# Performance work log

Hardware: AMD Instinct MI355X
Metric: run time of the kernel (lower is better)

The kernel has to match this reference:

```python
import jax, jax.numpy as jnp
import numpy as np

B, L, W = 64, 20, 48
D = W * W           # 2304, MoE input/output size (image_width**2)
E = 4               # num_experts
HID = 2 * D         # expert hidden size
K = 1               # top_k
LOSS_COEF = 1e-2


def _cv_squared(x):
    # torch: x.var() (unbiased) / (x.mean()**2 + eps)
    eps = 1e-10
    return jnp.var(x, ddof=1) / (jnp.mean(x) ** 2 + eps)


def _moe(x, w_gate, w1, b1, w2, b2):
    # Noisy top-k gating, inference path (train=False => clean logits, no noise).
    logits = x @ w_gate                                   # [B, E]
    top_logits, top_idx = jax.lax.top_k(logits, K + 1)    # min(k+1, E)
    topk_gates = jax.nn.softmax(top_logits[:, :K], axis=-1)
    gates = jnp.zeros_like(logits).at[
        jnp.arange(x.shape[0])[:, None], top_idx[:, :K]
    ].set(topk_gates)                                     # [B, E] sparse gates
    importance = gates.sum(0)
    load = (gates > 0).sum(0).astype(x.dtype)             # _gates_to_load
    aux = LOSS_COEF * (_cv_squared(importance) + _cv_squared(load))
    # Dense expert compute weighted by gates (same math as dispatch/combine).
    h = jax.nn.relu(jnp.einsum('bd,edh->beh', x, w1) + b1)      # [B,E,HID]
    y = jnp.einsum('beh,ehd->bed', h, w2) + b2                  # [B,E,D]
    out = jnp.einsum('be,bed->bd', gates, y)                    # [B,D]
    return out, aux


def _conv3d(x, w, b, pad):
    y = jax.lax.conv_general_dilated(
        x, w, window_strides=(1, 1, 1), padding=pad,
        dimension_numbers=('NCDHW', 'OIDHW', 'NCDHW'))
    return y + b[None, :, None, None, None]


def _forward(input, conv1_w, conv1_b, conv2_w, conv2_b,
             t_gate, t_w1, t_b1, t_w2, t_b2,
             a_gate, a_w1, a_b1, a_w2, a_b2,
             q_gate, q_w1, q_b1, q_w2, q_b2,
             enc_w, enc_b, dec_w, dec_b):
    x = jnp.transpose(input, (0, 2, 1, 3, 4))                   # [B,1,L,H,W]
    x = jax.nn.relu(_conv3d(x, conv1_w, conv1_b, ((1, 1), (1, 1), (1, 1))))
    x = jax.nn.relu(_conv3d(x, conv2_w, conv2_b, ((0, 0), (1, 1), (1, 1))))  # [B,1,1,H,W]
    xf = x.reshape(x.shape[0], -1)                              # [B, D]
    transform, l1 = _moe(xf, t_gate, t_w1, t_b1, t_w2, t_b2)
    add, l2 = _moe(xf, a_gate, a_w1, a_b1, a_w2, a_b2)
    quad, l3 = _moe(xf, q_gate, q_w1, q_b1, q_w2, q_b2)
    s = input.shape                                             # [B,L,1,H,W]
    transform = transform.reshape(s[0], 1, s[2], s[3], s[4])
    add = add.reshape(s[0], 1, s[2], s[3], s[4])
    quad = quad.reshape(s[0], 1, s[2], s[3], s[4])
    out = input * input * quad + input * transform + add        # [B,L,1,H,W]
    # encoder = Linear(D,D)+ReLU, decoder = Linear(D,D) over flattened H*W
    of = out.reshape(s[0], s[1], D)
    of = jax.nn.relu(of @ enc_w + enc_b)
    of = of @ dec_w + dec_b
    of = jax.nn.sigmoid(of)
    return of.reshape(s), l1 + l2 + l3


def setup_inputs() -> dict:
    key = jax.random.key(0)
    ks = jax.random.split(key, 32)
    sc = 0.02
    inp = {
        'input': jax.random.normal(ks[0], (B, L, 1, W, W), jnp.float32),
        'conv1_w': jax.random.normal(ks[1], (10, 1, 3, 3, 3), jnp.float32) * sc,
        'conv1_b': jnp.zeros((10,), jnp.float32),
        'conv2_w': jax.random.normal(ks[2], (1, 10, L, 3, 3), jnp.float32) * sc,
        'conv2_b': jnp.zeros((1,), jnp.float32),
        'enc_w': jax.random.normal(ks[3], (D, D), jnp.float32) * sc,
        'enc_b': jnp.zeros((D,), jnp.float32),
        'dec_w': jax.random.normal(ks[4], (D, D), jnp.float32) * sc,
        'dec_b': jnp.zeros((D,), jnp.float32),
    }
    for i, p in enumerate(['t', 'a', 'q']):
        k0, k1, k2 = jax.random.split(ks[5 + i], 3)
        inp[p + '_gate'] = jnp.zeros((D, E), jnp.float32) + jax.random.normal(k0, (D, E), jnp.float32) * sc
        inp[p + '_w1'] = jax.random.normal(k1, (E, D, HID), jnp.float32) * sc
        inp[p + '_b1'] = jnp.zeros((E, HID), jnp.float32)
        inp[p + '_w2'] = jax.random.normal(k2, (E, HID, D), jnp.float32) * sc
        inp[p + '_b2'] = jnp.zeros((E, D), jnp.float32)
    return inp


def reference(input, conv1_w, conv1_b, conv2_w, conv2_b,
              t_gate, t_w1, t_b1, t_w2, t_b2,
              a_gate, a_w1, a_b1, a_w2, a_b2,
              q_gate, q_w1, q_b1, q_w2, q_b2,
              enc_w, enc_b, dec_w, dec_b):
    return _forward(input, conv1_w, conv1_b, conv2_w, conv2_b,
                    t_gate, t_w1, t_b1, t_w2, t_b2,
                    a_gate, a_w1, a_b1, a_w2, a_b2,
                    q_gate, q_w1, q_b1, q_w2, q_b2,
                    enc_w, enc_b, dec_w, dec_b)
```

## Files before the change

kernel.cpp:

```cpp
#include <hip/hip_runtime.h>
#include <stdint.h>

#define NB 64
#define NL 20
#define ND 2304
#define NE 4
#define NH 4608
#define NM 1280

typedef float f32x4 __attribute__((ext_vector_type(4)));
typedef __bf16 bf16x8 __attribute__((ext_vector_type(8)));
typedef unsigned short u16;
typedef u16 u16x4 __attribute__((ext_vector_type(4)));
typedef unsigned int u32;
typedef u32 u32x4 __attribute__((ext_vector_type(4)));

__device__ __forceinline__ u16 f2bf(float f) {
  u32 u = __builtin_bit_cast(u32, f);
  u += 0x7fffu + ((u >> 16) & 1u);
  return (u16)(u >> 16);
}

__device__ __forceinline__ void gl_lds16(const void* g, void* l) {
  __builtin_amdgcn_global_load_lds(
      (const __attribute__((address_space(1))) void*)g,
      (__attribute__((address_space(3))) void*)l, 16, 0, 0);
}

#define OFF_XFACC 0
#define OFF_XF    147456
#define OFF_H     294912
#define OFF_Y     1179648
#define OFF_AUX   1622016
#define OFF_CNT   1622020
#define OFF_ROWS  1622032
#define OFF_OFB   1622240
#define OFF_H1B   3096800
#define OFF_ENCWB 4571360
#define OFF_DECWB 7225568
#define OFF_XC    9879776
#define OFF_P     10322144

__global__ __launch_bounds__(256) void k_zero(float* __restrict__ p) {
  p[(size_t)blockIdx.x * 256 + threadIdx.x] = 0.f;
}

__global__ __launch_bounds__(256) void k_conv(
    const float* __restrict__ in, const float* __restrict__ w1,
    const float* __restrict__ b1, const float* __restrict__ w2,
    float* __restrict__ xf_acc) {
  __shared__ float insl[3][50][50];
  __shared__ float c1[2][50][50];
  __shared__ float w1s[270];
  __shared__ float w2s[90];
  __shared__ float b1s[10];
  const int d = blockIdx.x, b = blockIdx.y, t = threadIdx.x;
  for (int i = t; i < 270; i += 256) w1s[i] = w1[i];
  for (int i = t; i < 90; i += 256) w2s[i] = w2[(size_t)((i / 9) * 20 + d) * 9 + (i % 9)];
  if (t < 10) b1s[t] = b1[t];
  for (int i = t; i < 7500; i += 256) {
    int s = i / 2500, rr = (i % 2500) / 50, cc = i % 50;
    int gd = d - 1 + s, gy = rr - 1, gx = cc - 1;
    float v = 0.f;
    if (gd >= 0 && gd < NL && (unsigned)gy < 48u && (unsigned)gx < 48u)
      v = in[((size_t)b * NL + gd) * ND + gy * 48 + gx];
    insl[s][rr][cc] = v;
  }
  for (int i = t; i < 5000; i += 256) ((float*)c1)[i] = 0.f;
  float s2[3][4];
#pragma unroll
  for (int qi = 0; qi < 3; ++qi)
#pragma unroll
    for (int xq = 0; xq < 4; ++xq) s2[qi][xq] = 0.f;
  __syncthreads();
  for (int pc = 0; pc < 5; ++pc) {
#pragma unroll
    for (int qi = 0; qi < 3; ++qi) {
      int q = t + qi * 256;
      if (q < 576) {
        int y = q / 12, x0 = (q % 12) * 4;
        float a0[4], a1[4];
        const float bb0 = b1s[2 * pc], bb1 = b1s[2 * pc + 1];
#pragma unroll
        for (int xq = 0; xq < 4; ++xq) { a0[xq] = bb0; a1[xq] = bb1; }
#pragma unroll
        for (int kd = 0; kd < 3; ++kd)
#pragma unroll
          for (int ky = 0; ky < 3; ++ky) {
            float v[6];
#pragma unroll
            for (int i = 0; i < 6; ++i) v[i] = insl[kd][y + ky][x0 + i];
            const float* wa = &w1s[(2 * pc) * 27 + kd * 9 + ky * 3];
            const float* wb = wa + 27;
#pragma unroll
            for (int xq = 0; xq < 4; ++xq) {
              a0[xq] += v[xq] * wa[0] + v[xq + 1] * wa[1] + v[xq + 2] * wa[2];
              a1[xq] += v[xq] * wb[0] + v[xq + 1] * wb[1] + v[xq + 2] * wb[2];
            }
          }
#pragma unroll
        for (int xq = 0; xq < 4; ++xq) {
          c1[0][y + 1][x0 + 1 + xq] = fmaxf(a0[xq], 0.f);
          c1[1][y + 1][x0 + 1 + xq] = fmaxf(a1[xq], 0.f);
        }
      }
    }
    __syncthreads();
#pragma unroll
    for (int qi = 0; qi < 3; ++qi) {
      int q = t + qi * 256;
      if (q < 576) {
        int y = q / 12, x0 = (q % 12) * 4;
#pragma unroll
        for (int cc = 0; cc < 2; ++cc) {
#pragma unroll
          for (int ky = 0; ky < 3; ++ky) {
            float v[6];
#pragma unroll
            for (int i = 0; i < 6; ++i) v[i] = c1[cc][y + ky][x0 + i];
            const float* wr = &w2s[(2 * pc + cc) * 9 + ky * 3];
#pragma unroll
            for (int xq = 0; xq < 4; ++xq)
              s2[qi][xq] += v[xq] * wr[0] + v[xq + 1] * wr[1] + v[xq + 2] * wr[2];
          }
        }
      }
    }
    __syncthreads();
  }
#pragma unroll
  for (int qi = 0; qi < 3; ++qi) {
    int q = t + qi * 256;
    if (q < 576) {
#pragma unroll
      for (int xq = 0; xq < 4; ++xq)
        atomicAdd(&xf_acc[(size_t)b * ND + q * 4 + xq], s2[qi][xq]);
    }
  }
}

__global__ __launch_bounds__(256) void k_bias_relu(
    const float* __restrict__ acc, const float* __restrict__ c2b, float* __restrict__ xf) {
  size_t i = (size_t)blockIdx.x * 256 + threadIdx.x;
  xf[i] = fmaxf(acc[i] + c2b[0], 0.f);
}

__global__ __launch_bounds__(256) void k_gate(
    const float* __restrict__ xf,
    const float* __restrict__ g0, const float* __restrict__ g1, const float* __restrict__ g2,
    float* __restrict__ aux, int* __restrict__ cnt, int* __restrict__ rows) {
  const int p = blockIdx.x, t = threadIdx.x;
  const float* __restrict__ g = (p == 0) ? g0 : ((p == 1) ? g1 : g2);
  __shared__ float lg[64][4];
  __shared__ int lidx[64];
  __shared__ int lcnt[4];
  if (t < 4) lcnt[t] = 0;
  const int wv = t >> 6, l = t & 63;
  for (int b0 = 0; b0 < 64; b0 += 4) {
    int bb = b0 + wv;
    f32x4 acc = {0.f, 0.f, 0.f, 0.f};
    const float* xr = xf + (size_t)bb * ND + l * 36;
    const float* gr = g + (size_t)l * 36 * 4;
#pragma unroll
    for (int i4 = 0; i4 < 9; ++i4) {
      f32x4 xv = *(const f32x4*)(xr + i4 * 4);
#pragma unroll
      for (int qq = 0; qq < 4; ++qq) {
        f32x4 gv = *(const f32x4*)(gr + (i4 * 4 + qq) * 4);
        acc += xv[qq] * gv;
      }
    }
#pragma unroll
    for (int e = 0; e < 4; ++e) {
      float pv = acc[e];
#pragma unroll
      for (int off = 32; off > 0; off >>= 1) pv += __shfl_down(pv, off);
      if (l == 0) lg[bb][e] = pv;
    }
  }
  __syncthreads();
  if (t < 64) {
    float best = lg[t][0];
    int bi = 0;
#pragma unroll
    for (int e = 1; e < 4; ++e)
      if (lg[t][e] > best) { best = lg[t][e]; bi = e; }
    lidx[t] = bi;
    atomicAdd(&lcnt[bi], 1);
  }
  __syncthreads();
  if (t == 0) {
    int ofs[4]; int run = 0;
#pragma unroll
    for (int e = 0; e < 4; ++e) { ofs[e] = run; run += lcnt[e]; cnt[p * 4 + e] = lcnt[e]; }
    for (int b = 0; b < 64; ++b) { int e = lidx[b]; rows[p * 64 + ofs[e]++] = b; }
    float var = 0.f;
#pragma unroll
    for (int e = 0; e < 4; ++e) { float dd = (float)lcnt[e] - 16.f; var += dd * dd; }
    var *= (1.f / 3.f);
    aux[p] = 0.02f * var / (256.f + 1e-10f);
  }
}

__global__ __launch_bounds__(256) void k_gather(
    const float* __restrict__ xf, const int* __restrict__ rows, u16* __restrict__ Xb) {
  const int slot = blockIdx.x, t = threadIdx.x;
  const int r = rows[slot];
  const f32x4* src = (const f32x4*)(xf + (size_t)r * ND);
  u16x4* dst = (u16x4*)(Xb + (size_t)slot * ND);
  for (int i = t; i < ND / 4; i += 256) {
    f32x4 v = src[i];
    u16x4 o;
#pragma unroll
    for (int q = 0; q < 4; ++q) o[q] = f2bf(v[q]);
    dst[i] = o;
  }
}

template <int K, int N, int KS>
__global__ __launch_bounds__(256) void k_moe_mfma(
    const u16* __restrict__ Xb,
    const float* __restrict__ wt, const float* __restrict__ wa, const float* __restrict__ wq,
    const int* __restrict__ cnt, float* __restrict__ P) {
  constexpr int KL = K / KS;
  constexpr int NT = KL / 32;
  const int tile = blockIdx.x;
  const int ks = blockIdx.y;
  const int pe = blockIdx.z >> 1, ch = blockIdx.z & 1;
  const int p = pe >> 2, e = pe & 3;
  const int c = cnt[p * 4 + e];
  const int rstart = ch * 32;
  if (rstart >= c) return;
  const int nrows = min(32, c - rstart);
  int pref = 0;
  for (int e2 = 0; e2 < e; ++e2) pref += cnt[p * 4 + e2];
  const int slot0 = p * 64 + pref + rstart;
  const float* __restrict__ W = (p == 0) ? wt : ((p == 1) ? wa : wq);
  __shared__ float wb[4][32 * 64];
  const int t = threadIdx.x;
  const int w = t >> 6, l = t & 63;
  const int l15 = l & 15, l4 = l >> 4;
  const int mbase = (w & 1) * 16;
  const int nb0 = (w >> 1) * 32;

  int ar = slot0 + mbase + l15; if (ar > 191) ar = 191;
  const u16* Ag = Xb + (size_t)ar * K + ks * KL + l4 * 8;
  bf16x8 areg[NT];
#pragma unroll
  for (int kt = 0; kt < NT; ++kt) areg[kt] = *(const bf16x8*)(Ag + kt * 32);

  const float* Wg = W + (size_t)e * K * N + (size_t)(ks * KL) * N + tile * 64;
#define STAGEW(BUF, KT)                                                       \
  { _Pragma("unroll")                                                         \
    for (int j = 0; j < 2; ++j)                                               \
      gl_lds16(Wg + ((size_t)((KT) * 32 + w * 8 + j * 4 + l4)) * N + l15 * 4, \
               &wb[BUF][(w * 8 + j * 4) * 64]); }

  f32x4 acc[2] = {};

  STAGEW(0, 0); STAGEW(1, 1); STAGEW(2, 2);
  asm volatile("s_waitcnt vmcnt(0)" ::: "memory");
  __syncthreads();

#pragma unroll
  for (int kt = 0; kt < NT; ++kt) {
    if (kt + 3 < NT) STAGEW((kt + 3) & 3, kt + 3);
    const float* ww = &wb[kt & 3][0];
#pragma unroll
    for (int i = 0; i < 2; ++i) {
      const int nb = nb0 + i * 16 + l15;
      bf16x8 bfr;
#pragma unroll
      for (int j = 0; j < 8; ++j)
        bfr[j] = (__bf16)ww[(l4 * 8 + j) * 64 + nb];
      acc[i] = __builtin_amdgcn_mfma_f32_16x16x32_bf16(areg[kt], bfr, acc[i], 0, 0, 0);
    }
    if (kt + 3 < NT)      { asm volatile("s_waitcnt vmcnt(4)" ::: "memory"); }
    else if (kt + 2 < NT) { asm volatile("s_waitcnt vmcnt(2)" ::: "memory"); }
    else if (kt + 1 < NT) { asm volatile("s_waitcnt vmcnt(0)" ::: "memory"); }
    __syncthreads();
  }
#undef STAGEW

  const size_t pbase = (size_t)ks * 192 * N;
#pragma unroll
  for (int i = 0; i < 2; ++i) {
    const int n = tile * 64 + nb0 + i * 16 + l15;
#pragma unroll
    for (int r = 0; r < 4; ++r) {
      const int m = mbase + l4 * 4 + r;
      if (m < nrows) P[pbase + (size_t)(slot0 + m) * N + n] = acc[i][r];
    }
  }
}

__global__ __launch_bounds__(256) void k_red1(
    const float* __restrict__ P,
    const float* __restrict__ b1t, const float* __restrict__ b1a, const float* __restrict__ b1q,
    const int* __restrict__ cnt, u16* __restrict__ Hb) {
  const int slot = blockIdx.y;
  const int p = slot >> 6, pos = slot & 63;
  int e = 0, run = cnt[p * 4];
  while (pos >= run && e < 3) { ++e; run += cnt[p * 4 + e]; }
  const float* __restrict__ b1 = (p == 0) ? b1t : ((p == 1) ? b1a : b1q);
  const int j0 = blockIdx.x * 1024 + threadIdx.x * 4;
  if (j0 >= NH) return;
  f32x4 s = *(const f32x4*)(b1 + (size_t)e * NH + j0);
#pragma unroll
  for (int ks = 0; ks < 8; ++ks)
    s += *(const f32x4*)(P + ((size_t)ks * 192 + slot) * NH + j0);
  u16x4 o;
#pragma unroll
  for (int q = 0; q < 4; ++q) o[q] = f2bf(fmaxf(s[q], 0.f));
  *(u16x4*)(Hb + (size_t)slot * NH + j0) = o;
}

__global__ __launch_bounds__(256) void k_red2(
    const float* __restrict__ P,
    const float* __restrict__ b2t, const float* __restrict__ b2a, const float* __restrict__ b2q,
    const int* __restrict__ cnt, const int* __restrict__ rows, float* __restrict__ Y) {
  const int slot = blockIdx.y;
  const int p = slot >> 6, pos = slot & 63;
  int e = 0, run = cnt[p * 4];
  while (pos >= run && e < 3) { ++e; run += cnt[p * 4 + e]; }
  const float* __restrict__ b2 = (p == 0) ? b2t : ((p == 1) ? b2a : b2q);
  const int b = rows[slot];
  const int t = threadIdx.x;
  if (t >= 192) return;
  const int j0 = blockIdx.x * 768 + t * 4;
  f32x4 s = *(const f32x4*)(b2 + (size_t)e * ND + j0);
#pragma unroll
  for (int ks = 0; ks < 16; ++ks)
    s += *(const f32x4*)(P + ((size_t)ks * 192 + slot) * ND + j0);
  *(f32x4*)(Y + (size_t)(p * 64 + b) * ND + j0) = s;
}

__global__ __launch_bounds__(256) void k_combine(
    const float* __restrict__ in, const float* __restrict__ Y, u16* __restrict__ ofb) {
  const size_t i = (size_t)blockIdx.x * 256 + threadIdx.x;
  const size_t e0 = i * 4;
  const int row = (int)(e0 / ND);
  const int d = (int)(e0 - (size_t)row * ND);
  const int b = row / NL;
  f32x4 v = *(const f32x4*)(in + e0);
  const size_t yb = (size_t)b * ND + d;
  f32x4 tt = *(const f32x4*)(Y + yb);
  f32x4 aa = *(const f32x4*)(Y + (size_t)64 * ND + yb);
  f32x4 qq = *(const f32x4*)(Y + (size_t)128 * ND + yb);
  u16x4 o;
#pragma unroll
  for (int q = 0; q < 4; ++q) {
    float f = v[q] * v[q] * qq[q] + v[q] * tt[q] + aa[q];
    o[q] = f2bf(f);
  }
  *(u16x4*)(ofb + e0) = o;
}

__global__ __launch_bounds__(256) void k_wt(
    const float* __restrict__ encw, const float* __restrict__ decw,
    u16* __restrict__ encb, u16* __restrict__ decb) {
  __shared__ float tl[32][33];
  const float* __restrict__ src = blockIdx.z ? decw : encw;
  u16* __restrict__ dst = blockIdx.z ? decb : encb;
  const int k0 = blockIdx.x * 32, n0 = blockIdx.y * 32;
  const int tx = threadIdx.x & 31, ty = threadIdx.x >> 5;
  for (int r = ty; r < 32; r += 8) tl[r][tx] = src[(size_t)(k0 + r) * ND + n0 + tx];
  __syncthreads();
  for (int r = ty; r < 32; r += 8) dst[(size_t)(n0 + r) * ND + k0 + tx] = f2bf(tl[tx][r]);
}

template <int MODE>
__global__ __launch_bounds__(256) void k_gemm(
    const u16* __restrict__ A, const u16* __restrict__ Bt,
    const float* __restrict__ bias, void* __restrict__ outp,
    const float* __restrict__ aux) {
  __shared__ u16 As[64 * 32];
  __shared__ u16 Bs[128 * 32];
  const int t = threadIdx.x;
  const int bm = blockIdx.x, bn = blockIdx.y;
  const int lane = t & 63;
  const int wr = (t >> 7) & 1, wc = (t >> 6) & 1;
  const int l15 = lane & 15, l4 = lane >> 4;
  f32x4 acc[2][4] = {};
  const int r0 = t >> 2, kc0 = (t & 3) * 8;
  const int r1 = (t + 256) >> 2, kc1 = ((t + 256) & 3) * 8;
  const size_t baseA = (size_t)(bm * 64) * ND;
  const size_t baseB = (size_t)(bn * 128) * ND;
  for (int k0 = 0; k0 < ND; k0 += 32) {
    *(u32x4*)(As + t * 8) = *(const u32x4*)(A + baseA + (size_t)r0 * ND + k0 + kc0);
    *(u32x4*)(Bs + t * 8) = *(const u32x4*)(Bt + baseB + (size_t)r0 * ND + k0 + kc0);
    *(u32x4*)(Bs + (t + 256) * 8) = *(const u32x4*)(Bt + baseB + (size_t)r1 * ND + k0 + kc1);
    __syncthreads();
    bf16x8 af[2], bfr[4];
#pragma unroll
    for (int i = 0; i < 2; ++i)
      af[i] = *(const bf16x8*)(As + (wr * 32 + i * 16 + l15) * 32 + l4 * 8);
#pragma unroll
    for (int i = 0; i < 4; ++i)
      bfr[i] = *(const bf16x8*)(Bs + (wc * 64 + i * 16 + l15) * 32 + l4 * 8);
#pragma unroll
    for (int mi = 0; mi < 2; ++mi)
#pragma unroll
      for (int ni = 0; ni < 4; ++ni)
        acc[mi][ni] = __builtin_amdgcn_mfma_f32_16x16x32_bf16(af[mi], bfr[ni], acc[mi][ni], 0, 0, 0);
    __syncthreads();
  }
  const int colbase = bn * 128 + wc * 64;
  const int rowbase = bm * 64 + wr * 32;
#pragma unroll
  for (int mi = 0; mi < 2; ++mi) {
#pragma unroll
    for (int ni = 0; ni < 4; ++ni) {
      const int colg = colbase + ni * 16 + l15;
      const float bv = bias[colg];
#pragma unroll
      for (int r = 0; r < 4; ++r) {
        const int rowg = rowbase + mi * 16 + l4 * 4 + r;
        float v = acc[mi][ni][r] + bv;
        if (MODE == 0) {
          ((u16*)outp)[(size_t)rowg * ND + colg] = f2bf(fmaxf(v, 0.f));
        } else {
          ((float*)outp)[(size_t)rowg * ND + colg] = 1.f / (1.f + __expf(-v));
        }
      }
    }
  }
  if (MODE == 1 && bm == 0 && bn == 0 && t == 0)
    ((float*)outp)[(size_t)NM * ND] = aux[0] + aux[1] + aux[2];
}

extern "C" void kernel_launch(void* const* d_in, const int* in_sizes, int n_in,
                              void* d_out, int out_size, void* d_ws, size_t ws_size,
                              hipStream_t stream) {
  (void)in_sizes; (void)n_in; (void)out_size; (void)ws_size;
  const float* input   = (const float*)d_in[0];
  const float* conv1_w = (const float*)d_in[1];
  const float* conv1_b = (const float*)d_in[2];
  const float* conv2_w = (const float*)d_in[3];
  const float* conv2_b = (const float*)d_in[4];
  const float* enc_w   = (const float*)d_in[5];
  const float* enc_b   = (const float*)d_in[6];
  const float* dec_w   = (const float*)d_in[7];
  const float* dec_b   = (const float*)d_in[8];
  const float* gate_t = (const float*)d_in[9];
  const float* w1_t   = (const float*)d_in[10];
  const float* b1_t   = (const float*)d_in[11];
  const float* w2_t   = (const float*)d_in[12];
  const float* b2_t   = (const float*)d_in[13];
  const float* gate_a = (const float*)d_in[14];
  const float* w1_a   = (const float*)d_in[15];
  const float* b1_a   = (const float*)d_in[16];
  const float* w2_a   = (const float*)d_in[17];
  const float* b2_a   = (const float*)d_in[18];
  const float* gate_q = (const float*)d_in[19];
  const float* w1_q   = (const float*)d_in[20];
  const float* b1_q   = (const float*)d_in[21];
  const float* w2_q   = (const float*)d_in[22];
  const float* b2_q   = (const float*)d_in[23];

  float* ws = (float*)d_ws;
  float* xf_acc = ws + OFF_XFACC;
  float* xf     = ws + OFF_XF;
  u16*   Hb     = (u16*)(ws + OFF_H);
  float* Y      = ws + OFF_Y;
  float* aux    = ws + OFF_AUX;
  int*   cnt    = (int*)(ws + OFF_CNT);
  int*   rows   = (int*)(ws + OFF_ROWS);
  u16*   ofb    = (u16*)(ws + OFF_OFB);
  u16*   h1b    = (u16*)(ws + OFF_H1B);
  u16*   encwb  = (u16*)(ws + OFF_ENCWB);
  u16*   decwb  = (u16*)(ws + OFF_DECWB);
  u16*   Xcb    = (u16*)(ws + OFF_XC);
  float* P      = ws + OFF_P;

  k_zero<<<576, 256, 0, stream>>>(xf_acc);
  k_conv<<<dim3(20, 64), 256, 0, stream>>>(input, conv1_w, conv1_b, conv2_w, xf_acc);
  k_bias_relu<<<576, 256, 0, stream>>>(xf_acc, conv2_b, xf);
  k_wt<<<dim3(72, 72, 2), 256, 0, stream>>>(enc_w, dec_w, encwb, decwb);
  k_gate<<<3, 256, 0, stream>>>(xf, gate_t, gate_a, gate_q, aux, cnt, rows);
  k_gather<<<192, 256, 0, stream>>>(xf, rows, Xcb);
  k_moe_mfma<ND, NH, 8><<<dim3(72, 8, 24), 256, 0, stream>>>(Xcb, w1_t, w1_a, w1_q, cnt, P);
  k_red1<<<dim3(5, 192), 256, 0, stream>>>(P, b1_t, b1_a, b1_q, cnt, Hb);
  k_moe_mfma<NH, ND, 16><<<dim3(36, 16, 24), 256, 0, stream>>>(Hb, w2_t, w2_a, w2_q, cnt, P);
  k_red2<<<dim3(3, 192), 256, 0, stream>>>(P, b2_t, b2_a, b2_q, cnt, rows, Y);
  k_combine<<<2880, 256, 0, stream>>>(input, Y, ofb);
  k_gemm<0><<<dim3(20, 18), 256, 0, stream>>>(ofb, encwb, enc_b, (void*)h1b, aux);
  k_gemm<1><<<dim3(20, 18), 256, 0, stream>>>(h1b, decwb, dec_b, d_out, aux);
}
```

Baseline: 527.0 us.

## Load MoE expert weights directly into registers instead of staging through LDS

Removes the LDS ring buffer and global_load_lds staging for the fp32 expert weights in the MoE MFMA kernel. Each lane now loads its own weight column values straight into registers with a two-buffer software prefetch. A-fragments are also loaded per iteration instead of being preloaded into a register array. This drops the LDS round trip and the per-step barriers and waitcnts. In exchange the global loads are scalar 4-byte loads with a large row stride, so coalescing is poorer, and the code assumes NT is odd.

```diff
diff --git a/kernel.cpp b/kernel.cpp
--- a/kernel.cpp
+++ b/kernel.cpp
@@ -19,12 +19,6 @@
   u32 u = __builtin_bit_cast(u32, f);
   u += 0x7fffu + ((u >> 16) & 1u);
   return (u16)(u >> 16);
-}
-
-__device__ __forceinline__ void gl_lds16(const void* g, void* l) {
-  __builtin_amdgcn_global_load_lds(
-      (const __attribute__((address_space(1))) void*)g,
-      (__attribute__((address_space(3))) void*)l, 16, 0, 0);
 }
 
 #define OFF_XFACC 0
@@ -236,7 +230,6 @@
   for (int e2 = 0; e2 < e; ++e2) pref += cnt[p * 4 + e2];
   const int slot0 = p * 64 + pref + rstart;
   const float* __restrict__ W = (p == 0) ? wt : ((p == 1) ? wa : wq);
-  __shared__ float wb[4][32 * 64];
   const int t = threadIdx.x;
   const int w = t >> 6, l = t & 63;
   const int l15 = l & 15, l4 = l >> 4;
@@ -245,42 +238,41 @@
 
   int ar = slot0 + mbase + l15; if (ar > 191) ar = 191;
   const u16* Ag = Xb + (size_t)ar * K + ks * KL + l4 * 8;
-  bf16x8 areg[NT];
-#pragma unroll
-  for (int kt = 0; kt < NT; ++kt) areg[kt] = *(const bf16x8*)(Ag + kt * 32);
-
-  const float* Wg = W + (size_t)e * K * N + (size_t)(ks * KL) * N + tile * 64;
-#define STAGEW(BUF, KT)                                                       \
+
+  const float* Wg = W + (size_t)e * K * N + (size_t)(ks * KL + l4 * 8) * N
+                      + tile * 64 + nb0 + l15;
+
+  float wA[16], wB[16];
+  f32x4 acc[2] = {};
+
+#define LOADW(BUF, KT)                                                        \
   { _Pragma("unroll")                                                         \
-    for (int j = 0; j < 2; ++j)                                               \
-      gl_lds16(Wg + ((size_t)((KT) * 32 + w * 8 + j * 4 + l4)) * N + l15 * 4, \
-               &wb[BUF][(w * 8 + j * 4) * 64]); }
-
-  f32x4 acc[2] = {};
-
-  STAGEW(0, 0); STAGEW(1, 1); STAGEW(2, 2);
-  asm volatile("s_waitcnt vmcnt(0)" ::: "memory");
-  __syncthreads();
-
-#pragma unroll
-  for (int kt = 0; kt < NT; ++kt) {
-    if (kt + 3 < NT) STAGEW((kt + 3) & 3, kt + 3);
-    const float* ww = &wb[kt & 3][0];
-#pragma unroll
-    for (int i = 0; i < 2; ++i) {
-      const int nb = nb0 + i * 16 + l15;
-      bf16x8 bfr;
-#pragma unroll
-      for (int j = 0; j < 8; ++j)
-        bfr[j] = (__bf16)ww[(l4 * 8 + j) * 64 + nb];
-      acc[i] = __builtin_amdgcn_mfma_f32_16x16x32_bf16(areg[kt], bfr, acc[i], 0, 0, 0);
-    }
-    if (kt + 3 < NT)      { asm volatile("s_waitcnt vmcnt(4)" ::: "memory"); }
-    else if (kt + 2 < NT) { asm volatile("s_waitcnt vmcnt(2)" ::: "memory"); }
-    else if (kt + 1 < NT) { asm volatile("s_waitcnt vmcnt(0)" ::: "memory"); }
-    __syncthreads();
-  }
-#undef STAGEW
+    for (int i = 0; i < 2; ++i)                                               \
+      _Pragma("unroll")                                                       \
+      for (int j = 0; j < 8; ++j)                                             \
+        BUF[i * 8 + j] = Wg[(size_t)((KT) * 32 + j) * N + i * 16]; }
+
+#define DO_MFMA(BUF, AF)                                                      \
+  { _Pragma("unroll")                                                         \
+    for (int i = 0; i < 2; ++i) {                                             \
+      bf16x8 bfr;                                                             \
+      _Pragma("unroll")                                                       \
+      for (int j = 0; j < 8; ++j) bfr[j] = (__bf16)BUF[i * 8 + j];            \
+      acc[i] = __builtin_amdgcn_mfma_f32_16x16x32_bf16(AF, bfr, acc[i], 0, 0, 0); \
+    } }
+
+  LOADW(wA, 0);
+#pragma unroll 1
+  for (int pr = 0; pr < (NT - 1) / 2; ++pr) {
+    const int kt = pr * 2;
+    LOADW(wB, kt + 1);
+    { bf16x8 a0 = *(const bf16x8*)(Ag + kt * 32); DO_MFMA(wA, a0); }
+    LOADW(wA, kt + 2);
+    { bf16x8 a1 = *(const bf16x8*)(Ag + (kt + 1) * 32); DO_MFMA(wB, a1); }
+  }
+  { bf16x8 a8 = *(const bf16x8*)(Ag + (NT - 1) * 32); DO_MFMA(wA, a8); }
+#undef LOADW
+#undef DO_MFMA
 
   const size_t pbase = (size_t)ks * 192 * N;
 #pragma unroll
```

Result: slower. 598.0 us (+13.5%).

## Replace conv atomics with per-depth partials and prefetch all MoE weight tiles

Applied to the files above, without the earlier changes.

The conv kernel now writes a separate partial sum for each depth slice into scratch, and the bias-relu kernel adds the 20 partials. This removes the zero-init kernel and the float atomics. The MoE MFMA kernel now issues every K-tile weight load up front into padded LDS buffers, one per tile, and waits on them one by one with decreasing vmcnt. This replaces the 4-deep ring buffer and removes the per-iteration restaging, in exchange for more LDS per block and a hardcoded wait sequence that assumes NT=9.

```diff
diff --git a/kernel.cpp b/kernel.cpp
--- a/kernel.cpp
+++ b/kernel.cpp
@@ -41,14 +41,10 @@
 #define OFF_XC    9879776
 #define OFF_P     10322144
 
-__global__ __launch_bounds__(256) void k_zero(float* __restrict__ p) {
-  p[(size_t)blockIdx.x * 256 + threadIdx.x] = 0.f;
-}
-
 __global__ __launch_bounds__(256) void k_conv(
     const float* __restrict__ in, const float* __restrict__ w1,
     const float* __restrict__ b1, const float* __restrict__ w2,
-    float* __restrict__ xf_acc) {
+    float* __restrict__ xfp) {
   __shared__ float insl[3][50][50];
   __shared__ float c1[2][50][50];
   __shared__ float w1s[270];
@@ -132,17 +128,19 @@
   for (int qi = 0; qi < 3; ++qi) {
     int q = t + qi * 256;
     if (q < 576) {
-#pragma unroll
-      for (int xq = 0; xq < 4; ++xq)
-        atomicAdd(&xf_acc[(size_t)b * ND + q * 4 + xq], s2[qi][xq]);
+      f32x4 o = {s2[qi][0], s2[qi][1], s2[qi][2], s2[qi][3]};
+      *(f32x4*)(xfp + ((size_t)d * NB + b) * ND + q * 4) = o;
     }
   }
 }
 
 __global__ __launch_bounds__(256) void k_bias_relu(
-    const float* __restrict__ acc, const float* __restrict__ c2b, float* __restrict__ xf) {
-  size_t i = (size_t)blockIdx.x * 256 + threadIdx.x;
-  xf[i] = fmaxf(acc[i] + c2b[0], 0.f);
+    const float* __restrict__ xfp, const float* __restrict__ c2b, float* __restrict__ xf) {
+  const size_t i = (size_t)blockIdx.x * 256 + threadIdx.x;
+  float s = c2b[0];
+#pragma unroll
+  for (int d = 0; d < NL; ++d) s += xfp[(size_t)d * (NB * ND) + i];
+  xf[i] = fmaxf(s, 0.f);
 }
 
 __global__ __launch_bounds__(256) void k_gate(
@@ -236,7 +234,7 @@
   for (int e2 = 0; e2 < e; ++e2) pref += cnt[p * 4 + e2];
   const int slot0 = p * 64 + pref + rstart;
   const float* __restrict__ W = (p == 0) ? wt : ((p == 1) ? wa : wq);
-  __shared__ float wb[4][32 * 64];
+  __shared__ float wb[NT][8 * 260];
   const int t = threadIdx.x;
   const int w = t >> 6, l = t & 63;
   const int l15 = l & 15, l4 = l >> 4;
@@ -250,37 +248,36 @@
   for (int kt = 0; kt < NT; ++kt) areg[kt] = *(const bf16x8*)(Ag + kt * 32);
 
   const float* Wg = W + (size_t)e * K * N + (size_t)(ks * KL) * N + tile * 64;
-#define STAGEW(BUF, KT)                                                       \
-  { _Pragma("unroll")                                                         \
-    for (int j = 0; j < 2; ++j)                                               \
-      gl_lds16(Wg + ((size_t)((KT) * 32 + w * 8 + j * 4 + l4)) * N + l15 * 4, \
-               &wb[BUF][(w * 8 + j * 4) * 64]); }
+#pragma unroll
+  for (int kt = 0; kt < NT; ++kt) {
+#pragma unroll
+    for (int j = 0; j < 2; ++j)
+      gl_lds16(Wg + ((size_t)(kt * 32 + w * 8 + j * 4 + l4)) * N + l15 * 4,
+               &wb[kt][(w * 2 + j) * 260]);
+  }
 
   f32x4 acc[2] = {};
 
-  STAGEW(0, 0); STAGEW(1, 1); STAGEW(2, 2);
-  asm volatile("s_waitcnt vmcnt(0)" ::: "memory");
-  __syncthreads();
-
-#pragma unroll
-  for (int kt = 0; kt < NT; ++kt) {
-    if (kt + 3 < NT) STAGEW((kt + 3) & 3, kt + 3);
-    const float* ww = &wb[kt & 3][0];
-#pragma unroll
-    for (int i = 0; i < 2; ++i) {
-      const int nb = nb0 + i * 16 + l15;
-      bf16x8 bfr;
-#pragma unroll
-      for (int j = 0; j < 8; ++j)
-        bfr[j] = (__bf16)ww[(l4 * 8 + j) * 64 + nb];
-      acc[i] = __builtin_amdgcn_mfma_f32_16x16x32_bf16(areg[kt], bfr, acc[i], 0, 0, 0);
-    }
-    if (kt + 3 < NT)      { asm volatile("s_waitcnt vmcnt(4)" ::: "memory"); }
-    else if (kt + 2 < NT) { asm volatile("s_waitcnt vmcnt(2)" ::: "memory"); }
-    else if (kt + 1 < NT) { asm volatile("s_waitcnt vmcnt(0)" ::: "memory"); }
-    __syncthreads();
-  }
-#undef STAGEW
+#define MOESTEP(KT, VM)                                                       \
+  {                                                                           \
+    asm volatile("s_waitcnt vmcnt(" #VM ")" ::: "memory");                    \
+    __syncthreads();                                                          \
+    const float* ww = &wb[KT][0];                                             \
+    _Pragma("unroll")                                                         \
+    for (int i = 0; i < 2; ++i) {                                             \
+      const int nb = nb0 + i * 16 + l15;                                      \
+      bf16x8 bfr;                                                             \
+      _Pragma("unroll")                                                       \
+      for (int jj = 0; jj < 8; ++jj)                                          \
+        bfr[jj] = (__bf16)ww[(l4 * 2 + (jj >> 2)) * 260 + (jj & 3) * 64 + nb];\
+      acc[i] = __builtin_amdgcn_mfma_f32_16x16x32_bf16(areg[KT], bfr, acc[i], 0, 0, 0); \
+    }                                                                         \
+  }
+
+  MOESTEP(0, 16); MOESTEP(1, 14); MOESTEP(2, 12); MOESTEP(3, 10);
+  MOESTEP(4, 8);  MOESTEP(5, 6);  MOESTEP(6, 4);  MOESTEP(7, 2);
+  MOESTEP(8, 0);
+#undef MOESTEP
 
   const size_t pbase = (size_t)ks * 192 * N;
 #pragma unroll
@@ -459,7 +456,6 @@
   const float* b2_q   = (const float*)d_in[23];
 
   float* ws = (float*)d_ws;
-  float* xf_acc = ws + OFF_XFACC;
   float* xf     = ws + OFF_XF;
   u16*   Hb     = (u16*)(ws + OFF_H);
   float* Y      = ws + OFF_Y;
@@ -473,9 +469,8 @@
   u16*   Xcb    = (u16*)(ws + OFF_XC);
   float* P      = ws + OFF_P;
 
-  k_zero<<<576, 256, 0, stream>>>(xf_acc);
-  k_conv<<<dim3(20, 64), 256, 0, stream>>>(input, conv1_w, conv1_b, conv2_w, xf_acc);
-  k_bias_relu<<<576, 256, 0, stream>>>(xf_acc, conv2_b, xf);
+  k_conv<<<dim3(20, 64), 256, 0, stream>>>(input, conv1_w, conv1_b, conv2_w, P);
+  k_bias_relu<<<576, 256, 0, stream>>>(P, conv2_b, xf);
   k_wt<<<dim3(72, 72, 2), 256, 0, stream>>>(enc_w, dec_w, encwb, decwb);
   k_gate<<<3, 256, 0, stream>>>(xf, gate_t, gate_a, gate_q, aux, cnt, rows);
   k_gather<<<192, 256, 0, stream>>>(xf, rows, Xcb);
```

Result: faster. 506.5 us (-3.9%).
